# Kernel tuning notes

Measured on AMD Instinct MI355X. Metric: run time of the kernel, lower is better.

## Reference

```python
import jax, jax.numpy as jnp
import numpy as np

MU = 0.9
IN_DIM = 1024
OUT_DIM = 8192
N = 8192


def setup_inputs() -> dict:
    key = jax.random.key(0)
    ks = jax.random.split(key, 8)
    stdv = 1.0 / np.sqrt(IN_DIM)
    inp = {
        "x": jax.random.normal(ks[0], (N, IN_DIM), dtype=jnp.float32),
        "x_ctx": jax.random.normal(ks[1], (N, IN_DIM), dtype=jnp.float32),
        "labels": jax.random.randint(ks[2], (N,), 0, OUT_DIM, dtype=jnp.int64),
        # classifier: uniform(-stdv, stdv), shape [output_dim, input_dim]
        "classifier": jax.random.uniform(ks[3], (OUT_DIM, IN_DIM), dtype=jnp.float32, minval=-stdv, maxval=stdv),
        # ctx_q = Linear(input_dim, output_dim - 1)  (na_att=False)
        "ctx_q_w": jax.random.uniform(ks[4], (OUT_DIM - 1, IN_DIM), dtype=jnp.float32, minval=-stdv, maxval=stdv),
        "ctx_q_b": jnp.zeros((OUT_DIM - 1,), dtype=jnp.float32),
        # word_g = Linear(input_dim, 1)
        "word_g_w": jax.random.uniform(ks[5], (1, IN_DIM), dtype=jnp.float32, minval=-stdv, maxval=stdv),
        "word_g_b": jnp.zeros((1,), dtype=jnp.float32),
        # registered buffers, initialized to zero as in __init__
        "history_input": jnp.zeros((OUT_DIM - 1, IN_DIM), dtype=jnp.float32),
        "history_count": jnp.zeros((OUT_DIM - 1,), dtype=jnp.int64),
    }
    return inp


def reference(x, x_ctx, labels, classifier, ctx_q_w, ctx_q_b, word_g_w, word_g_b,
              history_input, history_count):
    # ---- update_history: fused segment-mean EMA (replaces python loop over classes) ----
    xs = jax.lax.stop_gradient(x)  # .clone().detach() in torch
    sums = jax.ops.segment_sum(xs, labels, num_segments=OUT_DIM)          # [C, D]
    cnts = jax.ops.segment_sum(jnp.ones((N,), xs.dtype), labels, num_segments=OUT_DIM)  # [C]
    means = sums / jnp.maximum(cnts, 1.0)[:, None]                        # per-class mean
    present = cnts[1:] > 0                                                # classes 1..C-1
    new_hist = jnp.where(present[:, None], MU * history_input + means[1:], history_input)
    new_count = history_count + present.astype(history_count.dtype)

    # ---- generate_substitute ----
    w_logits = x_ctx @ ctx_q_w.T + ctx_q_b                                # [N, C-1]
    w = jax.nn.softmax(w_logits, axis=-1)
    clamped = jnp.maximum(new_count, 1).astype(x.dtype)
    v = new_hist * (1.0 - MU) / (1.0 - jnp.power(MU, clamped))[:, None]   # bias-corrected EMA
    substitute = w @ v                                                    # [N, D]

    # ---- gated mix + classifier logits ----
    g = jax.nn.sigmoid(x @ word_g_w.T + word_g_b)                         # [N, 1]
    feat = g * x + (1.0 - g) * substitute
    logits = feat @ classifier.T                                          # [N, C]

    # ---- cross_entropy over labels >= 0 (masked mean, jit-safe) ----
    mask = labels >= 0
    logp = jax.nn.log_softmax(logits, axis=-1)
    safe_lbl = jnp.maximum(labels, 0)
    nll = -jnp.take_along_axis(logp, safe_lbl[:, None], axis=1)[:, 0]
    loss = jnp.sum(jnp.where(mask, nll, 0.0)) / jnp.maximum(jnp.sum(mask), 1).astype(nll.dtype)
    return loss, logits
```

## Files before the change

kernel.cpp:

```cpp
#include <hip/hip_runtime.h>
#include <hip/hip_bf16.h>
#include <cstddef>
#include <cstdint>

typedef __hip_bfloat16 bf16;
typedef float floatx4 __attribute__((ext_vector_type(4)));
typedef short shortx8 __attribute__((ext_vector_type(8)));

#define NROWS 8192
#define INDIM 1024
#define OUTDIM 8192
#define CM1 8191

__device__ __forceinline__ void gload16(const void* g, void* l) {
  __builtin_amdgcn_global_load_lds(
      (const __attribute__((address_space(1))) void*)g,
      (__attribute__((address_space(3))) void*)l, 16, 0, 0);
}

__global__ __launch_bounds__(256) void seg_acc_kernel(
    const float* __restrict__ x, const int* __restrict__ labels,
    float* __restrict__ sums, int* __restrict__ cnts) {
  int i = blockIdx.x;
  int l = labels[i];
  const float* xr = x + (size_t)i * INDIM;
  float* sr = sums + (size_t)l * INDIM;
  for (int d = threadIdx.x; d < INDIM; d += 256) atomicAdd(&sr[d], xr[d]);
  if (threadIdx.x == 0) atomicAdd(&cnts[l], 1);
}

__global__ __launch_bounds__(256) void cvt8_kernel(
    const float* __restrict__ in, bf16* __restrict__ out, long n_in, long n_out) {
  long i = ((long)blockIdx.x * 256 + threadIdx.x) * 8;
  if (i >= n_out) return;
  shortx8 o;
  if (i + 8 <= n_in) {
    floatx4 a = *(const floatx4*)(in + i);
    floatx4 b = *(const floatx4*)(in + i + 4);
#pragma unroll
    for (int j = 0; j < 4; j++) {
      o[j] = __builtin_bit_cast(short, __float2bfloat16(a[j]));
      o[j + 4] = __builtin_bit_cast(short, __float2bfloat16(b[j]));
    }
  } else {
#pragma unroll
    for (int j = 0; j < 8; j++) o[j] = 0;
  }
  *(shortx8*)(out + i) = o;
}

__global__ __launch_bounds__(256) void make_vt_kernel(
    const float* __restrict__ sums, const int* __restrict__ cnts,
    const float* __restrict__ hist, const int* __restrict__ hist_cnt,
    bf16* __restrict__ vT) {
  __shared__ float tile[64][65];
  __shared__ float scl[64];
  __shared__ float rc[64];
  __shared__ int prs[64];
  const int t = threadIdx.x;
  const int cb = blockIdx.x & 127;
  const int db = blockIdx.x >> 7;
  const int c0 = cb * 64, d0 = db * 64;

  if (t < 64) {
    int c = c0 + t;
    float scale = 0.f, rcnt = 0.f;
    int present = 0;
    if (c < CM1) {
      int cnt = cnts[c + 1];
      present = cnt > 0;
      rcnt = 1.0f / fmaxf((float)cnt, 1.0f);
      int nc = hist_cnt[c] + (present ? 1 : 0);
      float clamped = (float)(nc > 1 ? nc : 1);
      scale = 0.1f / (1.0f - powf(0.9f, clamped));
    }
    scl[t] = scale;
    rc[t] = rcnt;
    prs[t] = present;
  }
  __syncthreads();

  const int dl = t & 63;
  const int cl0 = t >> 6;
#pragma unroll
  for (int ii = 0; ii < 16; ii++) {
    int clc = cl0 * 16 + ii;
    int c = c0 + clc;
    float val = 0.f;
    if (c < CM1) {
      float mean = sums[(size_t)(c + 1) * INDIM + d0 + dl] * rc[clc];
      float h = hist[(size_t)c * INDIM + d0 + dl];
      float nh = prs[clc] ? (0.9f * h + mean) : h;
      val = nh * scl[clc];
    }
    tile[clc][dl] = val;
  }
  __syncthreads();

  const int clw = t & 63;
  const int dl0 = t >> 6;
#pragma unroll
  for (int jj = 0; jj < 16; jj++) {
    int dlc = dl0 * 16 + jj;
    vT[(size_t)(d0 + dlc) * OUTDIM + c0 + clw] = __float2bfloat16(tile[clw][dlc]);
  }
}

__device__ __forceinline__ void store_c(float* p, float v) { *p = v; }
__device__ __forceinline__ void store_c(bf16* p, float v) { *p = __float2bfloat16(v); }

template <typename OutT>
__global__ __launch_bounds__(256) void gemm_bt_kernel(
    const bf16* __restrict__ A, const bf16* __restrict__ B, OutT* __restrict__ C,
    int K, int ldc) {
  __shared__ bf16 As[128 * 64];
  __shared__ bf16 Bs[128 * 64];
  const int t = threadIdx.x;
  const int lane = t & 63;
  const int wave = t >> 6;

  const int bm = blockIdx.y * 128;
  const int bn = blockIdx.x * 128;

  const int wm = (wave >> 1) * 64;
  const int wn = (wave & 1) * 64;
  const int r = lane & 15;
  const int q = lane >> 4;
  const int wbase = t & 192;

  floatx4 acc[4][4];
#pragma unroll
  for (int i = 0; i < 4; i++)
#pragma unroll
    for (int j = 0; j < 4; j++) acc[i][j] = (floatx4){0.f, 0.f, 0.f, 0.f};

  for (int k0 = 0; k0 < K; k0 += 64) {
#pragma unroll
    for (int i = 0; i < 4; i++) {
      int c = t + i * 256;
      int row = c >> 3;
      int gc = ((c & 7) ^ (row & 7)) << 3;
      gload16(A + (size_t)(bm + row) * K + k0 + gc, &As[(i * 256 + wbase) * 8]);
      gload16(B + (size_t)(bn + row) * K + k0 + gc, &Bs[(i * 256 + wbase) * 8]);
    }
    __syncthreads();
#pragma unroll
    for (int kk = 0; kk < 64; kk += 32) {
      shortx8 af[4], bfr[4];
      const int pc = ((kk >> 3) + q) ^ (r & 7);
#pragma unroll
      for (int i = 0; i < 4; i++) {
        af[i] = *(const shortx8*)(&As[(wm + i * 16 + r) * 64 + pc * 8]);
        bfr[i] = *(const shortx8*)(&Bs[(wn + i * 16 + r) * 64 + pc * 8]);
      }
#pragma unroll
      for (int i = 0; i < 4; i++)
#pragma unroll
        for (int j = 0; j < 4; j++)
          acc[i][j] = __builtin_amdgcn_mfma_f32_16x16x32_bf16(af[i], bfr[j], acc[i][j], 0, 0, 0);
    }
    __syncthreads();
  }

#pragma unroll
  for (int i = 0; i < 4; i++)
#pragma unroll
    for (int j = 0; j < 4; j++)
#pragma unroll
      for (int rr = 0; rr < 4; rr++) {
        int m = bm + wm + i * 16 + q * 4 + rr;
        int n = bn + wn + j * 16 + r;
        store_c(&C[(size_t)m * ldc + n], acc[i][j][rr]);
      }
}

template <typename OutT>
__global__ __launch_bounds__(512) void gemm256_kernel(
    const bf16* __restrict__ A, const bf16* __restrict__ B, OutT* __restrict__ C,
    int K, int ldc) {
  __shared__ bf16 As[2][256 * 64];
  __shared__ bf16 Bs[2][256 * 64];
  const int t = threadIdx.x;
  const int lane = t & 63;
  const int wave = t >> 6;
  const int bm = blockIdx.y * 256;
  const int bn = blockIdx.x * 256;
  const int wr = (wave >> 2) * 128;
  const int wc = (wave & 3) * 64;
  const int r = lane & 15;
  const int q = lane >> 4;

  floatx4 acc[8][4];
#pragma unroll
  for (int i = 0; i < 8; i++)
#pragma unroll
    for (int j = 0; j < 4; j++) acc[i][j] = (floatx4){0.f, 0.f, 0.f, 0.f};

#define STAGE256(sel, kk0)                                                        \
  {                                                                               \
    _Pragma("unroll") for (int i = 0; i < 4; i++) {                               \
      int c = i * 512 + t;                                                        \
      int row = c >> 3;                                                           \
      int gc = ((c & 7) ^ (row & 7)) << 3;                                        \
      gload16(A + (size_t)(bm + row) * K + (kk0) + gc,                            \
              &As[sel][(i * 512 + wave * 64) * 8]);                               \
      gload16(B + (size_t)(bn + row) * K + (kk0) + gc,                            \
              &Bs[sel][(i * 512 + wave * 64) * 8]);                               \
    }                                                                             \
  }

#define COMPUTE256(sel)                                                           \
  {                                                                               \
    _Pragma("unroll") for (int kk = 0; kk < 64; kk += 32) {                       \
      shortx8 bfr[4];                                                             \
      _Pragma("unroll") for (int j = 0; j < 4; j++) {                             \
        int br = wc + j * 16 + r;                                                 \
        bfr[j] = *(const shortx8*)(&Bs[sel][br * 64 +                             \
                                           ((((kk >> 3) + q) ^ (br & 7)) << 3)]); \
      }                                                                           \
      _Pragma("unroll") for (int i = 0; i < 8; i++) {                             \
        int ar = wr + i * 16 + r;                                                 \
        shortx8 af = *(const shortx8*)(&As[sel][ar * 64 +                         \
                                           ((((kk >> 3) + q) ^ (ar & 7)) << 3)]); \
        _Pragma("unroll") for (int j = 0; j < 4; j++)                             \
          acc[i][j] =                                                             \
              __builtin_amdgcn_mfma_f32_16x16x32_bf16(af, bfr[j], acc[i][j], 0, 0, 0); \
      }                                                                           \
    }                                                                             \
  }

  const int nk = K >> 6;
  STAGE256(0, 0);
  __syncthreads();
  for (int kt = 0; kt < nk - 2; kt += 2) {
    STAGE256(1, (kt + 1) * 64);
    COMPUTE256(0);
    __syncthreads();
    STAGE256(0, (kt + 2) * 64);
    COMPUTE256(1);
    __syncthreads();
  }
  STAGE256(1, (nk - 1) * 64);
  COMPUTE256(0);
  __syncthreads();
  COMPUTE256(1);

  if constexpr (sizeof(OutT) == 2) {
    __syncthreads();
    bf16* slab = ((bf16*)As) + wave * 1024;
    const int lr = lane >> 2;
    const int lc = (lane & 3) * 16;
#pragma unroll
    for (int i = 0; i < 8; i++) {
#pragma unroll
      for (int j = 0; j < 4; j++)
#pragma unroll
        for (int rr = 0; rr < 4; rr++)
          slab[(q * 4 + rr) * 64 + j * 16 + r] = __float2bfloat16(acc[i][j][rr]);
      shortx8 v0 = *(const shortx8*)(&slab[lr * 64 + lc]);
      shortx8 v1 = *(const shortx8*)(&slab[lr * 64 + lc + 8]);
      OutT* crow = C + (size_t)(bm + wr + i * 16 + lr) * ldc + bn + wc + lc;
      *(shortx8*)crow = v0;
      *(shortx8*)(crow + 8) = v1;
    }
  } else {
#pragma unroll
    for (int i = 0; i < 8; i++)
#pragma unroll
      for (int j = 0; j < 4; j++)
#pragma unroll
        for (int rr = 0; rr < 4; rr++) {
          int m = bm + wr + i * 16 + q * 4 + rr;
          int n = bn + wc + j * 16 + r;
          C[(size_t)m * ldc + n] = acc[i][j][rr];
        }
  }
#undef STAGE256
#undef COMPUTE256
}

__global__ __launch_bounds__(256) void softmax_rows_kernel(
    bf16* __restrict__ wl, const float* __restrict__ bias) {
  __shared__ float red[4];
  const int t = threadIdx.x;
  bf16* p = wl + (size_t)blockIdx.x * OUTDIM;
  float vals[32];
  float mx = -1e30f;
#pragma unroll
  for (int i = 0; i < 32; i++) {
    int col = i * 256 + t;
    float v = -1e30f;
    if (col < CM1) v = __bfloat162float(p[col]) + bias[col];
    vals[i] = v;
    mx = fmaxf(mx, v);
  }
  for (int o = 32; o; o >>= 1) mx = fmaxf(mx, __shfl_down(mx, o, 64));
  if ((t & 63) == 0) red[t >> 6] = mx;
  __syncthreads();
  mx = fmaxf(fmaxf(red[0], red[1]), fmaxf(red[2], red[3]));
  __syncthreads();
  float s = 0.f;
#pragma unroll
  for (int i = 0; i < 32; i++) {
    int col = i * 256 + t;
    float e = (col < CM1) ? __expf(vals[i] - mx) : 0.f;
    vals[i] = e;
    s += e;
  }
  for (int o = 32; o; o >>= 1) s += __shfl_down(s, o, 64);
  if ((t & 63) == 0) red[t >> 6] = s;
  __syncthreads();
  s = red[0] + red[1] + red[2] + red[3];
  float rs = 1.0f / s;
#pragma unroll
  for (int i = 0; i < 32; i++) {
    int col = i * 256 + t;
    p[col] = __float2bfloat16(vals[i] * rs);
  }
}

__global__ __launch_bounds__(256) void g_feat_kernel(
    const float* __restrict__ x, const float* __restrict__ wg,
    const float* __restrict__ wgb, const bf16* __restrict__ sub,
    bf16* __restrict__ feat) {
  __shared__ float red[4];
  const int t = threadIdx.x;
  const float* xr = x + (size_t)blockIdx.x * INDIM;
  float dot = 0.f;
#pragma unroll
  for (int i = 0; i < 4; i++) {
    int d = i * 256 + t;
    dot += xr[d] * wg[d];
  }
  for (int o = 32; o; o >>= 1) dot += __shfl_down(dot, o, 64);
  if ((t & 63) == 0) red[t >> 6] = dot;
  __syncthreads();
  dot = red[0] + red[1] + red[2] + red[3];
  float g = 1.0f / (1.0f + __expf(-(dot + wgb[0])));
  const bf16* sr = sub + (size_t)blockIdx.x * INDIM;
  bf16* fr = feat + (size_t)blockIdx.x * INDIM;
#pragma unroll
  for (int i = 0; i < 4; i++) {
    int d = i * 256 + t;
    float f = g * xr[d] + (1.0f - g) * __bfloat162float(sr[d]);
    fr[d] = __float2bfloat16(f);
  }
}

__global__ __launch_bounds__(256) void ce_kernel(
    const float* __restrict__ logits, const int* __restrict__ labels,
    float* __restrict__ acc) {
  __shared__ float red[4];
  const int t = threadIdx.x;
  const float* p = logits + (size_t)blockIdx.x * OUTDIM;
  float vals[32];
  float mx = -1e30f;
#pragma unroll
  for (int i = 0; i < 32; i++) {
    float v = p[i * 256 + t];
    vals[i] = v;
    mx = fmaxf(mx, v);
  }
  for (int o = 32; o; o >>= 1) mx = fmaxf(mx, __shfl_down(mx, o, 64));
  if ((t & 63) == 0) red[t >> 6] = mx;
  __syncthreads();
  mx = fmaxf(fmaxf(red[0], red[1]), fmaxf(red[2], red[3]));
  __syncthreads();
  float s = 0.f;
#pragma unroll
  for (int i = 0; i < 32; i++) s += __expf(vals[i] - mx);
  for (int o = 32; o; o >>= 1) s += __shfl_down(s, o, 64);
  if ((t & 63) == 0) red[t >> 6] = s;
  __syncthreads();
  if (t == 0) {
    s = red[0] + red[1] + red[2] + red[3];
    int l = labels[blockIdx.x];
    if (l >= 0) {
      float nll = mx + logf(s) - p[l];
      atomicAdd(&acc[0], nll);
      atomicAdd(&acc[1], 1.0f);
    }
  }
}

__global__ void finalize_kernel(const float* __restrict__ acc, float* __restrict__ out) {
  out[0] = acc[0] / fmaxf(acc[1], 1.0f);
}

extern "C" void kernel_launch(void* const* d_in, const int* in_sizes, int n_in,
                              void* d_out, int out_size, void* d_ws, size_t ws_size,
                              hipStream_t stream) {
  const float* x        = (const float*)d_in[0];
  const float* x_ctx    = (const float*)d_in[1];
  const int*   labels   = (const int*)d_in[2];
  const float* cls      = (const float*)d_in[3];
  const float* ctxq_w   = (const float*)d_in[4];
  const float* ctxq_b   = (const float*)d_in[5];
  const float* wg_w     = (const float*)d_in[6];
  const float* wg_b     = (const float*)d_in[7];
  const float* hist     = (const float*)d_in[8];
  const int*   hist_cnt = (const int*)d_in[9];
  float* out = (float*)d_out;

  char* ws = (char*)d_ws;
  float* sums   = (float*)(ws + 0);
  int*   cnts   = (int*)  (ws + 33554432);
  float* acc    = (float*)(ws + 33587200);
  bf16* xctx_bf = (bf16*) (ws + 33587456);
  bf16* wq_bf   = (bf16*) (ws + 50364672);
  bf16* cls_bf  = (bf16*) (ws + 67141888);
  bf16* vT      = (bf16*) (ws + 83919104);
  bf16* wl      = (bf16*) (ws + 100696320);
  bf16* sub_bf  = (bf16*) (ws + 234914048);
  bf16* feat_bf = (bf16*) (ws + 251691264);

  hipMemsetAsync(ws, 0, 33587456 + 256, stream);

  seg_acc_kernel<<<NROWS, 256, 0, stream>>>(x, labels, sums, cnts);
  cvt8_kernel<<<4096, 256, 0, stream>>>(x_ctx, xctx_bf, (long)NROWS * INDIM,
                                        (long)NROWS * INDIM);
  cvt8_kernel<<<4096, 256, 0, stream>>>(ctxq_w, wq_bf, (long)CM1 * INDIM,
                                        (long)OUTDIM * INDIM);
  cvt8_kernel<<<4096, 256, 0, stream>>>(cls, cls_bf, (long)OUTDIM * INDIM,
                                        (long)OUTDIM * INDIM);
  make_vt_kernel<<<2048, 256, 0, stream>>>(sums, cnts, hist, hist_cnt, vT);

  gemm256_kernel<bf16><<<dim3(32, 32), 512, 0, stream>>>(xctx_bf, wq_bf, wl, 1024, OUTDIM);
  softmax_rows_kernel<<<NROWS, 256, 0, stream>>>(wl, ctxq_b);
  gemm_bt_kernel<bf16><<<dim3(8, 64), 256, 0, stream>>>(wl, vT, sub_bf, OUTDIM, INDIM);
  g_feat_kernel<<<NROWS, 256, 0, stream>>>(x, wg_w, wg_b, sub_bf, feat_bf);
  gemm256_kernel<float><<<dim3(32, 32), 512, 0, stream>>>(feat_bf, cls_bf, out + 1, 1024, OUTDIM);
  ce_kernel<<<NROWS, 256, 0, stream>>>(out + 1, labels, acc);
  finalize_kernel<<<1, 1, 0, stream>>>(acc, out);
}
```

Baseline: 1.180 ms.

## Fuse cross-entropy partial max/sum-exp into classifier GEMM epilogue

The classifier GEMM now computes per-row partial max and sum-of-exp for its 256-column tile in the epilogue and writes them to small buffers. A lightweight combine kernel merges the 32 partials per row and computes the NLL. This removes the separate pass that re-read the full fp32 logits matrix. In exchange it adds extra epilogue work and LDS syncs to the GEMM, and reuses part of the workspace for the partials.

```diff
diff --git a/kernel.cpp b/kernel.cpp
--- a/kernel.cpp
+++ b/kernel.cpp
@@ -174,10 +174,10 @@
       }
 }
 
-template <typename OutT>
+template <typename OutT, bool CE>
 __global__ __launch_bounds__(512) void gemm256_kernel(
     const bf16* __restrict__ A, const bf16* __restrict__ B, OutT* __restrict__ C,
-    int K, int ldc) {
+    int K, int ldc, float* __restrict__ pm, float* __restrict__ ps) {
   __shared__ bf16 As[2][256 * 64];
   __shared__ bf16 Bs[2][256 * 64];
   const int t = threadIdx.x;
@@ -275,8 +275,72 @@
           C[(size_t)m * ldc + n] = acc[i][j][rr];
         }
   }
+
+  if constexpr (CE) {
+    __syncthreads();
+    float* wmld = (float*)&As[0][0];
+    float* wsld = wmld + 1024;
+#pragma unroll
+    for (int i = 0; i < 8; i++) {
+#pragma unroll
+      for (int rr = 0; rr < 4; rr++) {
+        float m = fmaxf(fmaxf(acc[i][0][rr], acc[i][1][rr]),
+                        fmaxf(acc[i][2][rr], acc[i][3][rr]));
+#pragma unroll
+        for (int o = 1; o <= 8; o <<= 1) m = fmaxf(m, __shfl_xor(m, o, 64));
+        float s = 0.f;
+#pragma unroll
+        for (int j = 0; j < 4; j++) s += __expf(acc[i][j][rr] - m);
+#pragma unroll
+        for (int o = 1; o <= 8; o <<= 1) s += __shfl_xor(s, o, 64);
+        if (r == 0) {
+          int row = wr + i * 16 + q * 4 + rr;
+          wmld[row * 4 + (wave & 3)] = m;
+          wsld[row * 4 + (wave & 3)] = s;
+        }
+      }
+    }
+    __syncthreads();
+    if (t < 256) {
+      float m0 = wmld[t * 4], m1 = wmld[t * 4 + 1];
+      float m2 = wmld[t * 4 + 2], m3 = wmld[t * 4 + 3];
+      float M = fmaxf(fmaxf(m0, m1), fmaxf(m2, m3));
+      float S = wsld[t * 4] * __expf(m0 - M) + wsld[t * 4 + 1] * __expf(m1 - M) +
+                wsld[t * 4 + 2] * __expf(m2 - M) + wsld[t * 4 + 3] * __expf(m3 - M);
+      size_t idx = (size_t)(bm + t) * gridDim.x + blockIdx.x;
+      pm[idx] = M;
+      ps[idx] = S;
+    }
+  }
 #undef STAGE256
 #undef COMPUTE256
+}
+
+__global__ __launch_bounds__(64) void ce_combine_kernel(
+    const float* __restrict__ pm, const float* __restrict__ ps,
+    const float* __restrict__ logits, const int* __restrict__ labels,
+    float* __restrict__ acc) {
+  const int row = blockIdx.x;
+  const int l = threadIdx.x;
+  float m = -1e30f, s = 0.f;
+  if (l < 32) {
+    m = pm[(size_t)row * 32 + l];
+    s = ps[(size_t)row * 32 + l];
+  }
+  float M = m;
+#pragma unroll
+  for (int o = 1; o < 64; o <<= 1) M = fmaxf(M, __shfl_xor(M, o, 64));
+  float S = s * __expf(m - M);
+#pragma unroll
+  for (int o = 1; o < 64; o <<= 1) S += __shfl_xor(S, o, 64);
+  if (l == 0) {
+    int lbl = labels[row];
+    if (lbl >= 0) {
+      float nll = M + logf(S) - logits[(size_t)row * OUTDIM + lbl];
+      atomicAdd(&acc[0], nll);
+      atomicAdd(&acc[1], 1.0f);
+    }
+  }
 }
 
 __global__ __launch_bounds__(256) void softmax_rows_kernel(
@@ -344,42 +408,6 @@
     int d = i * 256 + t;
     float f = g * xr[d] + (1.0f - g) * __bfloat162float(sr[d]);
     fr[d] = __float2bfloat16(f);
-  }
-}
-
-__global__ __launch_bounds__(256) void ce_kernel(
-    const float* __restrict__ logits, const int* __restrict__ labels,
-    float* __restrict__ acc) {
-  __shared__ float red[4];
-  const int t = threadIdx.x;
-  const float* p = logits + (size_t)blockIdx.x * OUTDIM;
-  float vals[32];
-  float mx = -1e30f;
-#pragma unroll
-  for (int i = 0; i < 32; i++) {
-    float v = p[i * 256 + t];
-    vals[i] = v;
-    mx = fmaxf(mx, v);
-  }
-  for (int o = 32; o; o >>= 1) mx = fmaxf(mx, __shfl_down(mx, o, 64));
-  if ((t & 63) == 0) red[t >> 6] = mx;
-  __syncthreads();
-  mx = fmaxf(fmaxf(red[0], red[1]), fmaxf(red[2], red[3]));
-  __syncthreads();
-  float s = 0.f;
-#pragma unroll
-  for (int i = 0; i < 32; i++) s += __expf(vals[i] - mx);
-  for (int o = 32; o; o >>= 1) s += __shfl_down(s, o, 64);
-  if ((t & 63) == 0) red[t >> 6] = s;
-  __syncthreads();
-  if (t == 0) {
-    s = red[0] + red[1] + red[2] + red[3];
-    int l = labels[blockIdx.x];
-    if (l >= 0) {
-      float nll = mx + logf(s) - p[l];
-      atomicAdd(&acc[0], nll);
-      atomicAdd(&acc[1], 1.0f);
-    }
   }
 }
 
@@ -413,6 +441,8 @@
   bf16* wl      = (bf16*) (ws + 100696320);
   bf16* sub_bf  = (bf16*) (ws + 234914048);
   bf16* feat_bf = (bf16*) (ws + 251691264);
+  float* pm = (float*)(ws + 0);
+  float* ps = (float*)(ws + 1048576);
 
   hipMemsetAsync(ws, 0, 33587456 + 256, stream);
 
@@ -425,11 +455,13 @@
                                         (long)OUTDIM * INDIM);
   make_vt_kernel<<<2048, 256, 0, stream>>>(sums, cnts, hist, hist_cnt, vT);
 
-  gemm256_kernel<bf16><<<dim3(32, 32), 512, 0, stream>>>(xctx_bf, wq_bf, wl, 1024, OUTDIM);
+  gemm256_kernel<bf16, false><<<dim3(32, 32), 512, 0, stream>>>(
+      xctx_bf, wq_bf, wl, 1024, OUTDIM, nullptr, nullptr);
   softmax_rows_kernel<<<NROWS, 256, 0, stream>>>(wl, ctxq_b);
   gemm_bt_kernel<bf16><<<dim3(8, 64), 256, 0, stream>>>(wl, vT, sub_bf, OUTDIM, INDIM);
   g_feat_kernel<<<NROWS, 256, 0, stream>>>(x, wg_w, wg_b, sub_bf, feat_bf);
-  gemm256_kernel<float><<<dim3(32, 32), 512, 0, stream>>>(feat_bf, cls_bf, out + 1, 1024, OUTDIM);
-  ce_kernel<<<NROWS, 256, 0, stream>>>(out + 1, labels, acc);
+  gemm256_kernel<float, true><<<dim3(32, 32), 512, 0, stream>>>(
+      feat_bf, cls_bf, out + 1, 1024, OUTDIM, pm, ps);
+  ce_combine_kernel<<<NROWS, 64, 0, stream>>>(pm, ps, out + 1, labels, acc);
   finalize_kernel<<<1, 1, 0, stream>>>(acc, out);
 }
```

New measurement: 1.221 ms. 1.04x slower.
